# Performance work log

Measured on AMD Instinct MI355X. Metric: run time of the kernel, lower is better.

The kernel has to match this reference:

```python
import jax, jax.numpy as jnp
import numpy as np

B, N, D = 16, 8192, 64
M, S = 256, 32          # npoints, nsample
OUT = 128
RADIUS = 0.4
WC = 64                 # WeightNet output channels
BN_EPS = 1e-5
_BN_SCALE = 1.0 / np.sqrt(1.0 + BN_EPS)  # eval-mode BN, running mean 0 / var 1


def _bn(x, gamma, beta):
    shp = [1] * x.ndim
    shp[1] = -1
    return gamma.reshape(shp) * (x * _BN_SCALE) + beta.reshape(shp)


def _pdist2(a, b):
    # a (B,P,3), b (B,Q,3) -> (B,P,Q) squared distances
    return (jnp.sum(a * a, -1)[:, :, None] + jnp.sum(b * b, -1)[:, None, :]
            - 2.0 * jnp.einsum('bpd,bqd->bpq', a, b))


def _fps(xyz, npoints):
    # furthest point sampling, pointnet2 semantics (start at index 0)
    Bq, Nq, _ = xyz.shape
    first = jnp.zeros((Bq,), jnp.int32)

    def step(carry, _):
        dist, last = carry
        pt = xyz[jnp.arange(Bq), last]                   # (B,3)
        d = jnp.sum((xyz - pt[:, None, :]) ** 2, -1)
        dist = jnp.minimum(dist, d)
        nxt = jnp.argmax(dist, -1).astype(jnp.int32)
        return (dist, nxt), nxt

    init = (jnp.full((Bq, Nq), 1e10, xyz.dtype), first)
    _, rest = jax.lax.scan(step, init, None, length=npoints - 1)
    return jnp.concatenate([first[None], rest], 0).T     # (B, npoints)


def _ball_query(xyz, new_xyz, radius, nsample):
    # first `nsample` indices within radius, pad by repeating first valid index
    d2 = _pdist2(new_xyz, xyz)                           # (B,M,N)
    n = xyz.shape[1]
    key = jnp.where(d2 <= radius * radius, n - jnp.arange(n, dtype=jnp.int32), 0)
    vals, idx = jax.lax.top_k(key, nsample)              # lowest in-radius indices first
    return jnp.where(vals > 0, idx, idx[:, :, :1])


def _group(x_ch, idx):
    # x_ch (B,C,N), idx (B,M,S) -> (B,C,M,S)
    return jax.vmap(lambda f, i: f[:, i])(x_ch, idx)


def setup_inputs():
    key = jax.random.key(0)
    ks = jax.random.split(key, 8)
    f = jnp.float32

    def w(k, o, i):
        return (jax.random.normal(k, (o, i), f) / np.sqrt(i)).astype(f)

    return {
        'xyz': jax.random.uniform(ks[0], (B, N, 3), f),
        'feature': jax.random.normal(ks[1], (B, D, N), f),
        'w0': w(ks[2], WC, 3), 'b0': jnp.zeros((WC,), f), 'gamma0': jnp.ones((WC,), f), 'beta0': jnp.zeros((WC,), f),
        'w1': w(ks[3], WC, WC), 'b1': jnp.zeros((WC,), f), 'gamma1': jnp.ones((WC,), f), 'beta1': jnp.zeros((WC,), f),
        'w2': w(ks[4], WC, WC), 'b2': jnp.zeros((WC,), f),
        'wl': w(ks[5], OUT, D * WC), 'bl': jnp.zeros((OUT,), f), 'gammal': jnp.ones((OUT,), f), 'betal': jnp.zeros((OUT,), f),
        'wf': w(ks[6], OUT, D + OUT), 'bf': jnp.zeros((OUT,), f), 'gammaf': jnp.ones((OUT,), f), 'betaf': jnp.zeros((OUT,), f),
    }


def reference(xyz, feature, w0, b0, gamma0, beta0, w1, b1, gamma1, beta1, w2, b2,
              wl, bl, gammal, betal, wf, bf, gammaf, betaf):
    relu = jax.nn.relu
    # ---- furthest point sampling ----
    fidx = _fps(xyz, M)                                  # (B,M)
    new_xyz = xyz[jnp.arange(B)[:, None], fidx]          # (B,M,3)
    # ---- ball query + grouping ----
    gidx = _ball_query(xyz, new_xyz, RADIUS, S)          # (B,M,S)
    xyz_ch = jnp.transpose(xyz, (0, 2, 1))               # (B,3,N)
    grouped_xyz = _group(xyz_ch, gidx) - jnp.transpose(new_xyz, (0, 2, 1))[:, :, :, None]  # (B,3,M,S) centered
    grouped_feat = _group(feature, gidx)                 # (B,D,M,S)
    # ---- WeightNet (1x1 convs on offsets) ----
    h = relu(_bn(jnp.einsum('oc,bcms->boms', w0, grouped_xyz) + b0[None, :, None, None], gamma0, beta0))
    h = relu(_bn(jnp.einsum('oc,bcms->boms', w1, h) + b1[None, :, None, None], gamma1, beta1))
    weights = jnp.einsum('oc,bcms->boms', w2, h) + b2[None, :, None, None]  # (B,WC,M,S)
    # ---- weighted aggregation: (B,M,D,S) @ (B,M,S,WC) -> (B,M,D*WC) ----
    agg = jnp.einsum('bdms,bwms->bmdw', grouped_feat, weights).reshape(B, M, D * WC)
    new_feature = relu(_bn(jnp.einsum('od,bmd->bom', wl, agg) + bl[None, :, None], gammal, betal))  # (B,OUT,M)
    # ---- three-NN interpolation back to N points ----
    d2 = _pdist2(xyz, new_xyz)                           # (B,N,M)
    negd, nidx = jax.lax.top_k(-d2, 3)                   # 3 nearest sampled centers
    rd = 1.0 / (-negd + 1e-8)                            # reverse density on squared distance
    wts = rd / jnp.sum(rd, -1, keepdims=True)            # (B,N,3)
    gathered = jax.vmap(lambda f2, i: f2[:, i])(new_feature, nidx)  # (B,OUT,N,3)
    interp = jnp.einsum('bcnk,bnk->bcn', gathered, wts)  # (B,OUT,N)
    # ---- concat skip + final 1x1 conv ----
    cat = jnp.concatenate([interp, feature], 1)          # (B,OUT+D,N)
    return relu(_bn(jnp.einsum('oc,bcn->bon', wf, cat) + bf[None, :, None], gammaf, betaf))
```

## Files before the change

### kernel.cpp

```cpp
#include <hip/hip_runtime.h>
#include <hip/hip_bf16.h>
#include <cstdint>
#include <cstddef>

#define BB   16
#define NN   8192
#define DD   64
#define MM   256
#define SS   32
#define OUTC 128
#define WCC  64

using short8 = __attribute__((ext_vector_type(8))) short;
using f32x4  = __attribute__((ext_vector_type(4))) float;

__device__ __forceinline__ float bnf(float x, float g, float be){
    const float BNS = 0.99999500003749969f;
    return g * (x * BNS) + be;
}
__device__ __forceinline__ unsigned short f2bf(float f){
    __hip_bfloat16 h = __float2bfloat16(f);
    return *reinterpret_cast<unsigned short*>(&h);
}
__device__ __forceinline__ float bf2f(unsigned short u){
    return __uint_as_float(((unsigned)u) << 16);
}

#define PRE_GRID (16 + 2048 + 512 + 24)

__global__ __launch_bounds__(256, 1) void k_pre(const float* __restrict__ xyz, float* __restrict__ nxyz,
    const float* __restrict__ feature, unsigned short* __restrict__ featB,
    const float* __restrict__ wl, unsigned short* __restrict__ wlB,
    const float* __restrict__ wf, unsigned short* __restrict__ wfB){
  __shared__ union {
    struct {
      float sxyz[NN*3];
      float snew[MM*3];
      unsigned long long skey[2][4];
    } f;
    float tile[64][65];
  } sm;
  const int t = threadIdx.x;
  int blk = blockIdx.x;

  if (blk < 16){
    const int b = blk;
    const float* xb = xyz + (size_t)b*NN*3;
    for (int i = t; i < NN*3; i += 256) sm.f.sxyz[i] = xb[i];
    float px[32], py[32], pz[32], pn[32], dist[32];
#pragma unroll
    for (int i=0;i<32;i++){
      const int id = i*256 + t;
      px[i] = xb[id*3+0]; py[i] = xb[id*3+1]; pz[i] = xb[id*3+2];
      pn[i] = px[i]*px[i] + py[i]*py[i] + pz[i]*pz[i];
      dist[i] = 1e10f;
    }
    __syncthreads();
    float lx = sm.f.sxyz[0], ly = sm.f.sxyz[1], lz = sm.f.sxyz[2];
    if (t==0){ sm.f.snew[0]=lx; sm.f.snew[1]=ly; sm.f.snew[2]=lz; }
    for (int step=1; step<MM; ++step){
      const float nlx = -2.0f*lx, nly = -2.0f*ly, nlz = -2.0f*lz;
      const float l2s = lx*lx + ly*ly + lz*lz;
      float bv = 0.0f; int bil = 0;
#pragma unroll
      for (int i=0;i<32;i++){
        float c  = pn[i] + l2s;
        float d  = __builtin_fmaf(px[i], nlx, __builtin_fmaf(py[i], nly, __builtin_fmaf(pz[i], nlz, c)));
        float nd = fminf(dist[i], d);
        dist[i] = nd;
        bool gt = nd > bv;
        bv  = gt ? nd : bv;
        bil = gt ? i  : bil;
      }
      const int bi = bil*256 + t;
      unsigned long long key = ((unsigned long long)__float_as_uint(bv) << 32) | (unsigned)(NN-1 - bi);
#define DPP_U64_MAX(CTRL) do { \
        unsigned lo_ = (unsigned)key, hi_ = (unsigned)(key >> 32); \
        unsigned olo_ = (unsigned)__builtin_amdgcn_update_dpp((int)lo_, (int)lo_, (CTRL), 0xF, 0xF, 0); \
        unsigned ohi_ = (unsigned)__builtin_amdgcn_update_dpp((int)hi_, (int)hi_, (CTRL), 0xF, 0xF, 0); \
        unsigned long long ok_ = ((unsigned long long)ohi_ << 32) | olo_; \
        key = ok_ > key ? ok_ : key; \
      } while(0)
      DPP_U64_MAX(0x111);
      DPP_U64_MAX(0x112);
      DPP_U64_MAX(0x114);
      DPP_U64_MAX(0x118);
      DPP_U64_MAX(0x142);
      DPP_U64_MAX(0x143);
#undef DPP_U64_MAX
      {
        unsigned klo = (unsigned)__builtin_amdgcn_readlane((int)(unsigned)key, 63);
        unsigned khi = (unsigned)__builtin_amdgcn_readlane((int)(unsigned)(key >> 32), 63);
        key = ((unsigned long long)khi << 32) | klo;
      }
      const int p = step & 1;
      if ((t & 63) == 0) sm.f.skey[p][t>>6] = key;
      __syncthreads();
      unsigned long long k0=sm.f.skey[p][0], k1=sm.f.skey[p][1], k2=sm.f.skey[p][2], k3=sm.f.skey[p][3];
      unsigned long long ka = k0>k1?k0:k1, kb = k2>k3?k2:k3;
      unsigned long long kw = ka>kb?ka:kb;
      const int bid = (NN-1) - (int)(unsigned)(kw & 0xFFFFFFFFull);
      lx = sm.f.sxyz[bid*3+0]; ly = sm.f.sxyz[bid*3+1]; lz = sm.f.sxyz[bid*3+2];
      if (t==0){ sm.f.snew[step*3+0]=lx; sm.f.snew[step*3+1]=ly; sm.f.snew[step*3+2]=lz; }
    }
    __syncthreads();
    for (int i = t; i < MM*3; i += 256) nxyz[(size_t)b*MM*3 + i] = sm.f.snew[i];
    return;
  }
  blk -= 16;
  if (blk < 2048){
    const int b  = blk >> 7;
    const int n0 = (blk & 127) << 6;
    {
      const int d = t >> 2, j0 = (t & 3) << 4;
      const float* src = feature + ((size_t)b*DD + d)*NN + n0 + j0;
#pragma unroll
      for (int i=0;i<16;i+=4){
        float4 v = *(const float4*)(src + i);
        sm.tile[d][j0+i+0]=v.x; sm.tile[d][j0+i+1]=v.y; sm.tile[d][j0+i+2]=v.z; sm.tile[d][j0+i+3]=v.w;
      }
    }
    __syncthreads();
    {
      const int j = t >> 2, d0 = (t & 3) << 4;
      unsigned short hv[16];
#pragma unroll
      for (int i=0;i<16;i++) hv[i] = f2bf(sm.tile[d0+i][j]);
      unsigned short* dst = featB + ((size_t)b*NN + n0 + j)*64 + d0;
      *(uint4*)(dst)     = *(uint4*)(&hv[0]);
      *(uint4*)(dst + 8) = *(uint4*)(&hv[8]);
    }
    return;
  }
  blk -= 2048;
  if (blk < 512){
    int idx = (blk*256 + t)*4;
    float4 v = *(const float4*)(wl + idx);
    ushort4 h = make_ushort4(f2bf(v.x), f2bf(v.y), f2bf(v.z), f2bf(v.w));
    *(ushort4*)(wlB + idx) = h;
    return;
  }
  blk -= 512;
  {
    int idx = (blk*256 + t)*4;
    if (idx < 128*192){
      float4 v = *(const float4*)(wf + idx);
      ushort4 h = make_ushort4(f2bf(v.x), f2bf(v.y), f2bf(v.z), f2bf(v.w));
      *(ushort4*)(wfB + idx) = h;
    }
  }
}

__global__ __launch_bounds__(256) void k_group(const float* __restrict__ xyz,
    const float* __restrict__ nxyz,
    const float* __restrict__ w0, const float* __restrict__ b0,
    const float* __restrict__ g0, const float* __restrict__ be0,
    const float* __restrict__ w1, const float* __restrict__ b1,
    const float* __restrict__ g1, const float* __restrict__ be1,
    const float* __restrict__ w2, const float* __restrict__ b2,
    const unsigned short* __restrict__ featB,
    unsigned short* __restrict__ aggB){
  const int bm = blockIdx.x;
  const int b  = bm >> 8;
  const int t  = threadIdx.x;
  const int c  = t & 63;
  const int wg = t >> 6;
  __shared__ int   wlist[4][SS];
  __shared__ int   wcnt[4];
  __shared__ int   sidx[SS];
  __shared__ float sgx[3][SS];
  __shared__ float sh0[SS][WCC];
  __shared__ float sh1[SS][WCC];
  __shared__ float swt[SS][WCC];

  const float w0r0 = w0[c*3+0], w0r1 = w0[c*3+1], w0r2 = w0[c*3+2];
  const float b0c=b0[c], g0c=g0[c], be0c=be0[c];
  const float b1c=b1[c], g1c=g1[c], be1c=be1[c], b2c=b2[c];
  float w1r[64], w2r[64];
#pragma unroll
  for (int i=0;i<16;i++){
    float4 v = *(const float4*)(w1 + c*64 + i*4);
    w1r[i*4+0]=v.x; w1r[i*4+1]=v.y; w1r[i*4+2]=v.z; w1r[i*4+3]=v.w;
    float4 u = *(const float4*)(w2 + c*64 + i*4);
    w2r[i*4+0]=u.x; w2r[i*4+1]=u.y; w2r[i*4+2]=u.z; w2r[i*4+3]=u.w;
  }
  const float cx = nxyz[bm*3+0], cy = nxyz[bm*3+1], cz = nxyz[bm*3+2];
  const float* xb = xyz + (size_t)b*NN*3;
  const float R2 = (float)(0.4*0.4);

  {
    int cnt = 0;
    const int base = wg*2048;
    for (int n0=0; n0<2048 && cnt<SS; n0+=64){
      int n = base + n0 + c;
      float dx = xb[n*3+0]-cx, dy = xb[n*3+1]-cy, dz = xb[n*3+2]-cz;
      float d2 = dx*dx+dy*dy+dz*dz;
      bool in = (d2 <= R2);
      unsigned long long mk = __ballot(in);
      int rank = cnt + (int)__popcll(mk & ((1ull<<c)-1ull));
      if (in && rank < SS) wlist[wg][rank] = n;
      cnt += (int)__popcll(mk);
    }
    if (c==0) wcnt[wg] = min(cnt, SS);
  }
  __syncthreads();
  if (t < SS){
    const int c0=wcnt[0], c1=wcnt[1], c2=wcnt[2], c3=wcnt[3];
    const int a1=c0+c1, a2=a1+c2, a3=a2+c3;
    int idx;
    if      (t < c0) idx = wlist[0][t];
    else if (t < a1) idx = wlist[1][t-c0];
    else if (t < a2) idx = wlist[2][t-a1];
    else if (t < a3) idx = wlist[3][t-a2];
    else idx = (c0>0) ? wlist[0][0] : (c1>0) ? wlist[1][0] : (c2>0) ? wlist[2][0] : wlist[3][0];
    sidx[t] = idx;
    sgx[0][t] = xb[idx*3+0]-cx;
    sgx[1][t] = xb[idx*3+1]-cy;
    sgx[2][t] = xb[idx*3+2]-cz;
  }
  __syncthreads();
#pragma unroll
  for (int i=0;i<8;i++){
    const int s = i*4 + wg;
    float pre = w0r0*sgx[0][s] + w0r1*sgx[1][s] + w0r2*sgx[2][s] + b0c;
    sh0[s][c] = fmaxf(bnf(pre, g0c, be0c), 0.f);
  }
  __syncthreads();
#pragma unroll
  for (int i=0;i<8;i++){
    const int s = i*4 + wg;
    float a = b1c;
#pragma unroll
    for (int k=0;k<64;k+=4){
      float4 h = *(const float4*)(&sh0[s][k]);
      a += w1r[k]*h.x + w1r[k+1]*h.y + w1r[k+2]*h.z + w1r[k+3]*h.w;
    }
    sh1[s][c] = fmaxf(bnf(a, g1c, be1c), 0.f);
  }
  __syncthreads();
#pragma unroll
  for (int i=0;i<8;i++){
    const int s = i*4 + wg;
    float a = b2c;
#pragma unroll
    for (int k=0;k<64;k+=4){
      float4 h = *(const float4*)(&sh1[s][k]);
      a += w2r[k]*h.x + w2r[k+1]*h.y + w2r[k+2]*h.z + w2r[k+3]*h.w;
    }
    swt[s][c] = a;
  }
  __syncthreads();
  const int d = c;
  float acc[16];
#pragma unroll
  for (int j=0;j<16;j++) acc[j]=0.f;
  const unsigned short* fb = featB + (size_t)b*NN*64;
  for (int s=0;s<SS;s++){
    float fv = bf2f(fb[(size_t)sidx[s]*64 + d]);
#pragma unroll
    for (int j=0;j<16;j++) acc[j] += fv * swt[s][wg*16+j];
  }
  unsigned short h[16];
#pragma unroll
  for (int j=0;j<16;j++) h[j] = f2bf(acc[j]);
  unsigned short* ab = aggB + (size_t)bm*4096 + d*64 + wg*16;
  *(uint4*)(ab)     = *(uint4*)(&h[0]);
  *(uint4*)(ab + 8) = *(uint4*)(&h[8]);
}

__global__ __launch_bounds__(256) void k_nf_part(const unsigned short* __restrict__ aggB,
                                                 const unsigned short* __restrict__ wlB,
                                                 float* __restrict__ part){
  const int blk = blockIdx.x;
  const int rb  = blk >> 3;
  const int ks  = blk & 7;
  const int wid = threadIdx.x >> 6, lane = threadIdx.x & 63;
  const int m0 = rb*64 + wid*16;
  const int r  = lane & 15, kg = lane >> 4;
  f32x4 acc[8];
#pragma unroll
  for (int i=0;i<8;i++) acc[i] = (f32x4){0.f,0.f,0.f,0.f};
  const short* arow = (const short*)aggB + (size_t)(m0 + r)*4096 + ks*512 + kg*8;
  const short* brow = (const short*)wlB  + (size_t)r*4096        + ks*512 + kg*8;
#pragma unroll 4
  for (int kc=0; kc<16; kc++){
    short8 a = *(const short8*)(arow + kc*32);
#pragma unroll
    for (int ot=0; ot<8; ot++){
      short8 bfr = *(const short8*)(brow + (size_t)ot*16*4096 + kc*32);
      acc[ot] = __builtin_amdgcn_mfma_f32_16x16x32_bf16(a, bfr, acc[ot], 0, 0, 0);
    }
  }
  float* pb = part + ((size_t)ks << 19);
#pragma unroll
  for (int ot=0; ot<8; ot++){
#pragma unroll
    for (int rr=0; rr<4; rr++){
      int row = m0 + kg*4 + rr;
      pb[(size_t)row*128 + ot*16 + r] = acc[ot][rr];
    }
  }
}

__global__ __launch_bounds__(256) void k_nf_ep(const float* __restrict__ part,
    const float* __restrict__ bl, const float* __restrict__ gl, const float* __restrict__ bel,
    float* __restrict__ nfT){
  const int gid = blockIdx.x*256 + threadIdx.x;
  const int base = gid*4;
  const int o0 = base & 127;
  float sum[4] = {0.f, 0.f, 0.f, 0.f};
#pragma unroll
  for (int s=0;s<8;s++){
    float4 v = *(const float4*)(part + ((size_t)s<<19) + base);
    sum[0]+=v.x; sum[1]+=v.y; sum[2]+=v.z; sum[3]+=v.w;
  }
  float ov[4];
#pragma unroll
  for (int j=0;j<4;j++){
    const int o = o0 + j;
    ov[j] = fmaxf(bnf(sum[j] + bl[o], gl[o], bel[o]), 0.f);
  }
  *(float4*)(nfT + base) = make_float4(ov[0],ov[1],ov[2],ov[3]);
}

__global__ __launch_bounds__(256) void k_final(const float* __restrict__ xyz,
    const float* __restrict__ nxyz, const float* __restrict__ nfT,
    const unsigned short* __restrict__ featB, const unsigned short* __restrict__ wfB,
    const float* __restrict__ bf, const float* __restrict__ gf, const float* __restrict__ bef,
    float* __restrict__ out){
  const int blk = blockIdx.x;
  const int b  = blk >> 6;
  const int n0 = (blk & 63) << 7;
  __shared__ float snew[MM*3];
  __shared__ float sw[128][3];
  __shared__ int   si[128][3];
  const int t = threadIdx.x;
  if (t < 192){
    float4 v = *(const float4*)(nxyz + (size_t)b*MM*3 + t*4);
    snew[t*4+0]=v.x; snew[t*4+1]=v.y; snew[t*4+2]=v.z; snew[t*4+3]=v.w;
  }
  __syncthreads();
  if (t < 128){
    const int n = n0 + t;
    const float x = xyz[((size_t)b*NN+n)*3+0];
    const float y = xyz[((size_t)b*NN+n)*3+1];
    const float z = xyz[((size_t)b*NN+n)*3+2];
    float d1=1e30f, d2=1e30f, d3=1e30f; int i1=0,i2=0,i3=0;
    for (int m=0;m<MM;m++){
      float dx=x-snew[m*3+0], dy=y-snew[m*3+1], dz=z-snew[m*3+2];
      float d = dx*dx+dy*dy+dz*dz;
      if (d < d3){
        if (d < d1){ d3=d2;i3=i2; d2=d1;i2=i1; d1=d;i1=m; }
        else if (d < d2){ d3=d2;i3=i2; d2=d;i2=m; }
        else { d3=d;i3=m; }
      }
    }
    float r1=1.f/(d1+1e-8f), r2=1.f/(d2+1e-8f), r3=1.f/(d3+1e-8f);
    float rs = 1.f/(r1+r2+r3);
    sw[t][0]=r1*rs; sw[t][1]=r2*rs; sw[t][2]=r3*rs;
    si[t][0]=i1; si[t][1]=i2; si[t][2]=i3;
  }
  __syncthreads();

  const int w = t >> 6, lane = t & 63;
  const int r = lane & 15, kg = lane >> 4;
  float wA[8][3]; int iA[8][3];
#pragma unroll
  for (int nt=0;nt<8;nt++){
    int n = nt*16 + r;
    wA[nt][0]=sw[n][0]; wA[nt][1]=sw[n][1]; wA[nt][2]=sw[n][2];
    iA[nt][0]=si[n][0]*128; iA[nt][1]=si[n][1]*128; iA[nt][2]=si[n][2]*128;
  }
  const float* nfb = nfT + (size_t)b*MM*128;
  const unsigned short* fbB = featB + ((size_t)b*NN + n0)*64;
  const unsigned short* wfRow0 = wfB + (size_t)(w*32 +      r)*192 + kg*8;
  const unsigned short* wfRow1 = wfB + (size_t)(w*32 + 16 + r)*192 + kg*8;
  f32x4 acc[2][8];
#pragma unroll
  for (int i=0;i<2;i++)
#pragma unroll
    for (int j=0;j<8;j++) acc[i][j] = (f32x4){0.f,0.f,0.f,0.f};

#pragma unroll
  for (int c=0;c<6;c++){
    short8 a0 = *(const short8*)(wfRow0 + c*32);
    short8 a1 = *(const short8*)(wfRow1 + c*32);
    if (c < 4){
      const int k8 = c*32 + kg*8;
#pragma unroll
      for (int nt=0;nt<8;nt++){
        const float* p0 = nfb + iA[nt][0] + k8;
        const float* p1 = nfb + iA[nt][1] + k8;
        const float* p2 = nfb + iA[nt][2] + k8;
        float4 xa = *(const float4*)(p0), xb4 = *(const float4*)(p0+4);
        float4 ya = *(const float4*)(p1), yb4 = *(const float4*)(p1+4);
        float4 za = *(const float4*)(p2), zb4 = *(const float4*)(p2+4);
        const float w0v=wA[nt][0], w1v=wA[nt][1], w2v=wA[nt][2];
        float e0 = w0v*xa.x + w1v*ya.x + w2v*za.x;
        float e1 = w0v*xa.y + w1v*ya.y + w2v*za.y;
        float e2 = w0v*xa.z + w1v*ya.z + w2v*za.z;
        float e3 = w0v*xa.w + w1v*ya.w + w2v*za.w;
        float e4 = w0v*xb4.x + w1v*yb4.x + w2v*zb4.x;
        float e5 = w0v*xb4.y + w1v*yb4.y + w2v*zb4.y;
        float e6 = w0v*xb4.z + w1v*yb4.z + w2v*zb4.z;
        float e7 = w0v*xb4.w + w1v*yb4.w + w2v*zb4.w;
        short8 bfr = { (short)f2bf(e0), (short)f2bf(e1), (short)f2bf(e2), (short)f2bf(e3),
                       (short)f2bf(e4), (short)f2bf(e5), (short)f2bf(e6), (short)f2bf(e7) };
        acc[0][nt] = __builtin_amdgcn_mfma_f32_16x16x32_bf16(a0, bfr, acc[0][nt], 0, 0, 0);
        acc[1][nt] = __builtin_amdgcn_mfma_f32_16x16x32_bf16(a1, bfr, acc[1][nt], 0, 0, 0);
      }
    } else {
      const int d8 = (c-4)*32 + kg*8;
#pragma unroll
      for (int nt=0;nt<8;nt++){
        short8 bfr = *(const short8*)(fbB + (size_t)(nt*16 + r)*64 + d8);
        acc[0][nt] = __builtin_amdgcn_mfma_f32_16x16x32_bf16(a0, bfr, acc[0][nt], 0, 0, 0);
        acc[1][nt] = __builtin_amdgcn_mfma_f32_16x16x32_bf16(a1, bfr, acc[1][nt], 0, 0, 0);
      }
    }
  }
#pragma unroll
  for (int ot=0; ot<2; ot++){
#pragma unroll
    for (int rr=0; rr<4; rr++){
      const int o = w*32 + ot*16 + kg*4 + rr;
      const float bfo = bf[o], gfo = gf[o], befo = bef[o];
      float* dst = out + ((size_t)b*OUTC + o)*NN + n0 + r;
#pragma unroll
      for (int nt=0;nt<8;nt++){
        float val = fmaxf(bnf(acc[ot][nt][rr] + bfo, gfo, befo), 0.f);
        dst[nt*16] = val;
      }
    }
  }
}

extern "C" void kernel_launch(void* const* d_in, const int* in_sizes, int n_in,
                              void* d_out, int out_size, void* d_ws, size_t ws_size,
                              hipStream_t stream){
  const float* xyz     = (const float*)d_in[0];
  const float* feature = (const float*)d_in[1];
  const float* w0  = (const float*)d_in[2];
  const float* b0  = (const float*)d_in[3];
  const float* g0  = (const float*)d_in[4];
  const float* be0 = (const float*)d_in[5];
  const float* w1  = (const float*)d_in[6];
  const float* b1  = (const float*)d_in[7];
  const float* g1  = (const float*)d_in[8];
  const float* be1 = (const float*)d_in[9];
  const float* w2  = (const float*)d_in[10];
  const float* b2  = (const float*)d_in[11];
  const float* wl  = (const float*)d_in[12];
  const float* bl  = (const float*)d_in[13];
  const float* gl  = (const float*)d_in[14];
  const float* bel = (const float*)d_in[15];
  const float* wf  = (const float*)d_in[16];
  const float* bf  = (const float*)d_in[17];
  const float* gf  = (const float*)d_in[18];
  const float* bef = (const float*)d_in[19];
  float* out = (float*)d_out;

  char* ws = (char*)d_ws;
  unsigned short* featB = (unsigned short*)(ws + 0);
  float*          part  = (float*)(ws + 16777216);
  unsigned short* aggB  = (unsigned short*)(ws + 50331648);
  unsigned short* wlB   = (unsigned short*)(ws + 83886080);
  unsigned short* wfB   = (unsigned short*)(ws + 84934656);
  float*          nxyz  = (float*)(ws + 84983808);
  float*          nfT   = (float*)(ws + 85557248);

  k_pre    <<<PRE_GRID, 256, 0, stream>>>(xyz, nxyz, feature, featB, wl, wlB, wf, wfB);
  k_group  <<<BB*MM, 256, 0, stream>>>(xyz, nxyz, w0,b0,g0,be0, w1,b1,g1,be1, w2,b2, featB, aggB);
  k_nf_part<<<512,  256, 0, stream>>>(aggB, wlB, part);
  k_nf_ep  <<<512,  256, 0, stream>>>(part, bl, gl, bel, nfT);
  k_final  <<<BB*(NN/128), 256, 0, stream>>>(xyz, nxyz, nfT, featB, wfB, bf, gf, bef, out);
}
```

Baseline: 565.3 us.

## Fuse grouping into FPS kernel as persistent blocks overlapping via flag sync

Merges the k_group work into k_pre, launched as a persistent grid of 256 blocks. Sixteen blocks run FPS and publish sampled centers in 64-point chunks through release flags. The other 240 blocks first convert features and weights to bf16, then loop over grouping tasks, spinning on per-batch flags and feature-conversion counters. The aim is to hide the serial FPS latency behind feature conversion and grouping, and to drop a kernel launch. The cost is cross-block spin-waits that rely on all 256 blocks being co-resident, fewer blocks doing the grouping, and an extra zeroing kernel.

```diff
diff --git a/kernel.cpp b/kernel.cpp
--- a/kernel.cpp
+++ b/kernel.cpp
@@ -26,12 +26,21 @@
     return __uint_as_float(((unsigned)u) << 16);
 }
 
-#define PRE_GRID (16 + 2048 + 512 + 24)
+__global__ __launch_bounds__(64) void k_zero(int* __restrict__ syncw){
+  if (threadIdx.x < 32) syncw[threadIdx.x] = 0;
+}
 
 __global__ __launch_bounds__(256, 1) void k_pre(const float* __restrict__ xyz, float* __restrict__ nxyz,
     const float* __restrict__ feature, unsigned short* __restrict__ featB,
     const float* __restrict__ wl, unsigned short* __restrict__ wlB,
-    const float* __restrict__ wf, unsigned short* __restrict__ wfB){
+    const float* __restrict__ wf, unsigned short* __restrict__ wfB,
+    const float* __restrict__ w0, const float* __restrict__ b0,
+    const float* __restrict__ g0, const float* __restrict__ be0,
+    const float* __restrict__ w1, const float* __restrict__ b1,
+    const float* __restrict__ g1, const float* __restrict__ be1,
+    const float* __restrict__ w2, const float* __restrict__ b2,
+    unsigned short* __restrict__ aggB,
+    int* __restrict__ flags , int* __restrict__ tdone ){
   __shared__ union {
     struct {
       float sxyz[NN*3];
@@ -39,9 +48,18 @@
       unsigned long long skey[2][4];
     } f;
     float tile[64][65];
+    struct {
+      int   wlist[4][SS];
+      int   wcnt[4];
+      int   sidx[SS];
+      float sgx[3][SS];
+      float sh0[SS][WCC];
+      float sh1[SS][WCC];
+      float swt[SS][WCC];
+    } g;
   } sm;
   const int t = threadIdx.x;
-  int blk = blockIdx.x;
+  const int blk = blockIdx.x;
 
   if (blk < 16){
     const int b = blk;
@@ -102,77 +120,68 @@
       const int bid = (NN-1) - (int)(unsigned)(kw & 0xFFFFFFFFull);
       lx = sm.f.sxyz[bid*3+0]; ly = sm.f.sxyz[bid*3+1]; lz = sm.f.sxyz[bid*3+2];
       if (t==0){ sm.f.snew[step*3+0]=lx; sm.f.snew[step*3+1]=ly; sm.f.snew[step*3+2]=lz; }
-    }
-    __syncthreads();
-    for (int i = t; i < MM*3; i += 256) nxyz[(size_t)b*MM*3 + i] = sm.f.snew[i];
+      if ((step & 63) == 63 && step != MM-1){
+        __syncthreads();
+        const int chunk = step >> 6;
+        for (int i=t; i<192; i+=256) nxyz[(size_t)b*768 + chunk*192 + i] = sm.f.snew[chunk*192 + i];
+        __threadfence();
+        __syncthreads();
+        if (t==0) __hip_atomic_store(&flags[b], chunk+1, __ATOMIC_RELEASE, __HIP_MEMORY_SCOPE_AGENT);
+      }
+    }
+    __syncthreads();
+    for (int i=t; i<192; i+=256) nxyz[(size_t)b*768 + 576 + i] = sm.f.snew[576 + i];
+    __threadfence();
+    __syncthreads();
+    if (t==0) __hip_atomic_store(&flags[b], 4, __ATOMIC_RELEASE, __HIP_MEMORY_SCOPE_AGENT);
     return;
   }
-  blk -= 16;
-  if (blk < 2048){
-    const int b  = blk >> 7;
-    const int n0 = (blk & 127) << 6;
-    {
-      const int d = t >> 2, j0 = (t & 3) << 4;
-      const float* src = feature + ((size_t)b*DD + d)*NN + n0 + j0;
-#pragma unroll
-      for (int i=0;i<16;i+=4){
-        float4 v = *(const float4*)(src + i);
-        sm.tile[d][j0+i+0]=v.x; sm.tile[d][j0+i+1]=v.y; sm.tile[d][j0+i+2]=v.z; sm.tile[d][j0+i+3]=v.w;
-      }
-    }
-    __syncthreads();
-    {
-      const int j = t >> 2, d0 = (t & 3) << 4;
-      unsigned short hv[16];
-#pragma unroll
-      for (int i=0;i<16;i++) hv[i] = f2bf(sm.tile[d0+i][j]);
-      unsigned short* dst = featB + ((size_t)b*NN + n0 + j)*64 + d0;
-      *(uint4*)(dst)     = *(uint4*)(&hv[0]);
-      *(uint4*)(dst + 8) = *(uint4*)(&hv[8]);
-    }
-    return;
-  }
-  blk -= 2048;
-  if (blk < 512){
-    int idx = (blk*256 + t)*4;
-    float4 v = *(const float4*)(wl + idx);
-    ushort4 h = make_ushort4(f2bf(v.x), f2bf(v.y), f2bf(v.z), f2bf(v.w));
-    *(ushort4*)(wlB + idx) = h;
-    return;
-  }
-  blk -= 512;
-  {
-    int idx = (blk*256 + t)*4;
-    if (idx < 128*192){
-      float4 v = *(const float4*)(wf + idx);
+
+  const int wb = blk - 16;
+  for (int task = wb; task < 2048+512+24; task += 240){
+    if (task < 2048){
+      const int b  = task >> 7;
+      const int n0 = (task & 127) << 6;
+      {
+        const int d = t >> 2, j0 = (t & 3) << 4;
+        const float* src = feature + ((size_t)b*DD + d)*NN + n0 + j0;
+#pragma unroll
+        for (int i=0;i<16;i+=4){
+          float4 v = *(const float4*)(src + i);
+          sm.tile[d][j0+i+0]=v.x; sm.tile[d][j0+i+1]=v.y; sm.tile[d][j0+i+2]=v.z; sm.tile[d][j0+i+3]=v.w;
+        }
+      }
+      __syncthreads();
+      {
+        const int j = t >> 2, d0 = (t & 3) << 4;
+        unsigned short hv[16];
+#pragma unroll
+        for (int i=0;i<16;i++) hv[i] = f2bf(sm.tile[d0+i][j]);
+        unsigned short* dst = featB + ((size_t)b*NN + n0 + j)*64 + d0;
+        *(uint4*)(dst)     = *(uint4*)(&hv[0]);
+        *(uint4*)(dst + 8) = *(uint4*)(&hv[8]);
+      }
+      __threadfence();
+      __syncthreads();
+      if (t==0) __hip_atomic_fetch_add(&tdone[b], 1, __ATOMIC_RELEASE, __HIP_MEMORY_SCOPE_AGENT);
+      __syncthreads();
+    } else if (task < 2048+512){
+      int idx = (task-2048)*1024 + t*4;
+      float4 v = *(const float4*)(wl + idx);
       ushort4 h = make_ushort4(f2bf(v.x), f2bf(v.y), f2bf(v.z), f2bf(v.w));
-      *(ushort4*)(wfB + idx) = h;
-    }
-  }
-}
-
-__global__ __launch_bounds__(256) void k_group(const float* __restrict__ xyz,
-    const float* __restrict__ nxyz,
-    const float* __restrict__ w0, const float* __restrict__ b0,
-    const float* __restrict__ g0, const float* __restrict__ be0,
-    const float* __restrict__ w1, const float* __restrict__ b1,
-    const float* __restrict__ g1, const float* __restrict__ be1,
-    const float* __restrict__ w2, const float* __restrict__ b2,
-    const unsigned short* __restrict__ featB,
-    unsigned short* __restrict__ aggB){
-  const int bm = blockIdx.x;
-  const int b  = bm >> 8;
-  const int t  = threadIdx.x;
+      *(ushort4*)(wlB + idx) = h;
+    } else {
+      int idx = (task-2048-512)*1024 + t*4;
+      if (idx < 128*192){
+        float4 v = *(const float4*)(wf + idx);
+        ushort4 h = make_ushort4(f2bf(v.x), f2bf(v.y), f2bf(v.z), f2bf(v.w));
+        *(ushort4*)(wfB + idx) = h;
+      }
+    }
+  }
+
   const int c  = t & 63;
   const int wg = t >> 6;
-  __shared__ int   wlist[4][SS];
-  __shared__ int   wcnt[4];
-  __shared__ int   sidx[SS];
-  __shared__ float sgx[3][SS];
-  __shared__ float sh0[SS][WCC];
-  __shared__ float sh1[SS][WCC];
-  __shared__ float swt[SS][WCC];
-
   const float w0r0 = w0[c*3+0], w0r1 = w0[c*3+1], w0r2 = w0[c*3+2];
   const float b0c=b0[c], g0c=g0[c], be0c=be0[c];
   const float b1c=b1[c], g1c=g1[c], be1c=be1[c], b2c=b2[c];
@@ -184,88 +193,101 @@
     float4 u = *(const float4*)(w2 + c*64 + i*4);
     w2r[i*4+0]=u.x; w2r[i*4+1]=u.y; w2r[i*4+2]=u.z; w2r[i*4+3]=u.w;
   }
-  const float cx = nxyz[bm*3+0], cy = nxyz[bm*3+1], cz = nxyz[bm*3+2];
-  const float* xb = xyz + (size_t)b*NN*3;
   const float R2 = (float)(0.4*0.4);
 
-  {
-    int cnt = 0;
-    const int base = wg*2048;
-    for (int n0=0; n0<2048 && cnt<SS; n0+=64){
-      int n = base + n0 + c;
-      float dx = xb[n*3+0]-cx, dy = xb[n*3+1]-cy, dz = xb[n*3+2]-cz;
-      float d2 = dx*dx+dy*dy+dz*dz;
-      bool in = (d2 <= R2);
-      unsigned long long mk = __ballot(in);
-      int rank = cnt + (int)__popcll(mk & ((1ull<<c)-1ull));
-      if (in && rank < SS) wlist[wg][rank] = n;
-      cnt += (int)__popcll(mk);
-    }
-    if (c==0) wcnt[wg] = min(cnt, SS);
-  }
-  __syncthreads();
-  if (t < SS){
-    const int c0=wcnt[0], c1=wcnt[1], c2=wcnt[2], c3=wcnt[3];
-    const int a1=c0+c1, a2=a1+c2, a3=a2+c3;
-    int idx;
-    if      (t < c0) idx = wlist[0][t];
-    else if (t < a1) idx = wlist[1][t-c0];
-    else if (t < a2) idx = wlist[2][t-a1];
-    else if (t < a3) idx = wlist[3][t-a2];
-    else idx = (c0>0) ? wlist[0][0] : (c1>0) ? wlist[1][0] : (c2>0) ? wlist[2][0] : wlist[3][0];
-    sidx[t] = idx;
-    sgx[0][t] = xb[idx*3+0]-cx;
-    sgx[1][t] = xb[idx*3+1]-cy;
-    sgx[2][t] = xb[idx*3+2]-cz;
-  }
-  __syncthreads();
-#pragma unroll
-  for (int i=0;i<8;i++){
-    const int s = i*4 + wg;
-    float pre = w0r0*sgx[0][s] + w0r1*sgx[1][s] + w0r2*sgx[2][s] + b0c;
-    sh0[s][c] = fmaxf(bnf(pre, g0c, be0c), 0.f);
-  }
-  __syncthreads();
-#pragma unroll
-  for (int i=0;i<8;i++){
-    const int s = i*4 + wg;
-    float a = b1c;
-#pragma unroll
-    for (int k=0;k<64;k+=4){
-      float4 h = *(const float4*)(&sh0[s][k]);
-      a += w1r[k]*h.x + w1r[k+1]*h.y + w1r[k+2]*h.z + w1r[k+3]*h.w;
-    }
-    sh1[s][c] = fmaxf(bnf(a, g1c, be1c), 0.f);
-  }
-  __syncthreads();
-#pragma unroll
-  for (int i=0;i<8;i++){
-    const int s = i*4 + wg;
-    float a = b2c;
-#pragma unroll
-    for (int k=0;k<64;k+=4){
-      float4 h = *(const float4*)(&sh1[s][k]);
-      a += w2r[k]*h.x + w2r[k+1]*h.y + w2r[k+2]*h.z + w2r[k+3]*h.w;
-    }
-    swt[s][c] = a;
-  }
-  __syncthreads();
-  const int d = c;
-  float acc[16];
-#pragma unroll
-  for (int j=0;j<16;j++) acc[j]=0.f;
-  const unsigned short* fb = featB + (size_t)b*NN*64;
-  for (int s=0;s<SS;s++){
-    float fv = bf2f(fb[(size_t)sidx[s]*64 + d]);
-#pragma unroll
-    for (int j=0;j<16;j++) acc[j] += fv * swt[s][wg*16+j];
-  }
-  unsigned short h[16];
-#pragma unroll
-  for (int j=0;j<16;j++) h[j] = f2bf(acc[j]);
-  unsigned short* ab = aggB + (size_t)bm*4096 + d*64 + wg*16;
-  *(uint4*)(ab)     = *(uint4*)(&h[0]);
-  *(uint4*)(ab + 8) = *(uint4*)(&h[8]);
+  for (int T = wb; T < 4096; T += 240){
+    const int chunk = T >> 10;
+    const int i1k   = T & 1023;
+    const int b     = i1k & 15;
+    const int m     = chunk*64 + (i1k >> 4);
+    const int bm    = b*256 + m;
+    while (__hip_atomic_load(&flags[b], __ATOMIC_ACQUIRE, __HIP_MEMORY_SCOPE_AGENT) < chunk+1)
+      __builtin_amdgcn_s_sleep(8);
+    while (__hip_atomic_load(&tdone[b], __ATOMIC_ACQUIRE, __HIP_MEMORY_SCOPE_AGENT) < 128)
+      __builtin_amdgcn_s_sleep(8);
+
+    const float cx = nxyz[bm*3+0], cy = nxyz[bm*3+1], cz = nxyz[bm*3+2];
+    const float* xb = xyz + (size_t)b*NN*3;
+    {
+      int cnt = 0;
+      const int base = wg*2048;
+      for (int n0=0; n0<2048 && cnt<SS; n0+=64){
+        int n = base + n0 + c;
+        float dx = xb[n*3+0]-cx, dy = xb[n*3+1]-cy, dz = xb[n*3+2]-cz;
+        float d2 = dx*dx+dy*dy+dz*dz;
+        bool in = (d2 <= R2);
+        unsigned long long mk = __ballot(in);
+        int rank = cnt + (int)__popcll(mk & ((1ull<<c)-1ull));
+        if (in && rank < SS) sm.g.wlist[wg][rank] = n;
+        cnt += (int)__popcll(mk);
+      }
+      if (c==0) sm.g.wcnt[wg] = min(cnt, SS);
+    }
+    __syncthreads();
+    if (t < SS){
+      const int c0=sm.g.wcnt[0], c1=sm.g.wcnt[1], c2=sm.g.wcnt[2], c3=sm.g.wcnt[3];
+      const int a1=c0+c1, a2=a1+c2, a3=a2+c3;
+      int idx;
+      if      (t < c0) idx = sm.g.wlist[0][t];
+      else if (t < a1) idx = sm.g.wlist[1][t-c0];
+      else if (t < a2) idx = sm.g.wlist[2][t-a1];
+      else if (t < a3) idx = sm.g.wlist[3][t-a2];
+      else idx = (c0>0) ? sm.g.wlist[0][0] : (c1>0) ? sm.g.wlist[1][0] : (c2>0) ? sm.g.wlist[2][0] : sm.g.wlist[3][0];
+      sm.g.sidx[t] = idx;
+      sm.g.sgx[0][t] = xb[idx*3+0]-cx;
+      sm.g.sgx[1][t] = xb[idx*3+1]-cy;
+      sm.g.sgx[2][t] = xb[idx*3+2]-cz;
+    }
+    __syncthreads();
+#pragma unroll
+    for (int i=0;i<8;i++){
+      const int s = i*4 + wg;
+      float pre = w0r0*sm.g.sgx[0][s] + w0r1*sm.g.sgx[1][s] + w0r2*sm.g.sgx[2][s] + b0c;
+      sm.g.sh0[s][c] = fmaxf(bnf(pre, g0c, be0c), 0.f);
+    }
+    __syncthreads();
+#pragma unroll
+    for (int i=0;i<8;i++){
+      const int s = i*4 + wg;
+      float a = b1c;
+#pragma unroll
+      for (int k=0;k<64;k+=4){
+        float4 h = *(const float4*)(&sm.g.sh0[s][k]);
+        a += w1r[k]*h.x + w1r[k+1]*h.y + w1r[k+2]*h.z + w1r[k+3]*h.w;
+      }
+      sm.g.sh1[s][c] = fmaxf(bnf(a, g1c, be1c), 0.f);
+    }
+    __syncthreads();
+#pragma unroll
+    for (int i=0;i<8;i++){
+      const int s = i*4 + wg;
+      float a = b2c;
+#pragma unroll
+      for (int k=0;k<64;k+=4){
+        float4 h = *(const float4*)(&sm.g.sh1[s][k]);
+        a += w2r[k]*h.x + w2r[k+1]*h.y + w2r[k+2]*h.z + w2r[k+3]*h.w;
+      }
+      sm.g.swt[s][c] = a;
+    }
+    __syncthreads();
+    const int d = c;
+    float acc[16];
+#pragma unroll
+    for (int j=0;j<16;j++) acc[j]=0.f;
+    const unsigned short* fb = featB + (size_t)b*NN*64;
+    for (int s=0;s<SS;s++){
+      float fv = bf2f(fb[(size_t)sm.g.sidx[s]*64 + d]);
+#pragma unroll
+      for (int j=0;j<16;j++) acc[j] += fv * sm.g.swt[s][wg*16+j];
+    }
+    unsigned short h[16];
+#pragma unroll
+    for (int j=0;j<16;j++) h[j] = f2bf(acc[j]);
+    unsigned short* ab = aggB + (size_t)bm*4096 + d*64 + wg*16;
+    *(uint4*)(ab)     = *(uint4*)(&h[0]);
+    *(uint4*)(ab + 8) = *(uint4*)(&h[8]);
+    __syncthreads();
+  }
 }
 
 __global__ __launch_bounds__(256) void k_nf_part(const unsigned short* __restrict__ aggB,
@@ -468,10 +490,14 @@
   unsigned short* wfB   = (unsigned short*)(ws + 84934656);
   float*          nxyz  = (float*)(ws + 84983808);
   float*          nfT   = (float*)(ws + 85557248);
-
-  k_pre    <<<PRE_GRID, 256, 0, stream>>>(xyz, nxyz, feature, featB, wl, wlB, wf, wfB);
-  k_group  <<<BB*MM, 256, 0, stream>>>(xyz, nxyz, w0,b0,g0,be0, w1,b1,g1,be1, w2,b2, featB, aggB);
-  k_nf_part<<<512,  256, 0, stream>>>(aggB, wlB, part);
-  k_nf_ep  <<<512,  256, 0, stream>>>(part, bl, gl, bel, nfT);
+  int*            syncw = (int*)  (ws + 87654400);
+  int*            flags = syncw;
+  int*            tdone = syncw + 16;
+
+  k_zero   <<<1,   64, 0, stream>>>(syncw);
+  k_pre    <<<256, 256, 0, stream>>>(xyz, nxyz, feature, featB, wl, wlB, wf, wfB,
+                                     w0,b0,g0,be0, w1,b1,g1,be1, w2,b2, aggB, flags, tdone);
+  k_nf_part<<<512, 256, 0, stream>>>(aggB, wlB, part);
+  k_nf_ep  <<<512, 256, 0, stream>>>(part, bl, gl, bel, nfT);
   k_final  <<<BB*(NN/128), 256, 0, stream>>>(xyz, nxyz, nfT, featB, wfB, bf, gf, bef, out);
 }
```

New measurement: 960.7 us. 1.7x slower.
